# Optimization experiments

Measured on AMD Instinct MI355X. Metric: run time of the kernel, lower is better.

The kernel has to match this reference:

```python
import jax, jax.numpy as jnp
import numpy as np

N_STATE = 1024
N_HEAD = 16
HEAD_DIM = N_STATE // N_HEAD
SEQLENS = [1024, 896, 768, 640, 512, 384, 896, 1024]  # sum = 6144
TOTAL = sum(SEQLENS)


def setup_inputs() -> dict:
    key = jax.random.key(0)
    ks = jax.random.split(key, 8)
    s = 0.02
    cu = jnp.asarray(np.concatenate([[0], np.cumsum(SEQLENS)]), dtype=jnp.int32)
    return {
        "x": jax.random.normal(ks[0], (TOTAL, N_STATE), jnp.float32),
        "cu_seqlens": cu,
        "Wq": jax.random.normal(ks[1], (N_STATE, N_STATE), jnp.float32) * s,
        "bq": jax.random.normal(ks[2], (N_STATE,), jnp.float32) * s,
        "Wk": jax.random.normal(ks[3], (N_STATE, N_STATE), jnp.float32) * s,
        "Wv": jax.random.normal(ks[4], (N_STATE, N_STATE), jnp.float32) * s,
        "bv": jax.random.normal(ks[5], (N_STATE,), jnp.float32) * s,
        "Wo": jax.random.normal(ks[6], (N_STATE, N_STATE), jnp.float32) * s,
        "bo": jax.random.normal(ks[7], (N_STATE,), jnp.float32) * s,
    }


def reference(x, cu_seqlens, Wq, bq, Wk, Wv, bv, Wo, bo):
    # cu_seqlens is a static (host) quantity in the original (used via .tolist())
    cu = np.asarray(jax.device_get(cu_seqlens))
    seqlens = cu[1:] - cu[:-1]
    B = len(seqlens)
    Lmax = int(seqlens.max())

    q = x @ Wq.T + bq              # [T, n_state]
    k = x @ Wk.T                   # key has no bias
    v = x @ Wv.T + bv

    # static pad/unpad index maps (honoring the ragged structure)
    ar = np.arange(Lmax)
    valid = ar[None, :] < seqlens[:, None]             # [B, Lmax]
    idx = np.where(valid, cu[:-1, None] + ar[None, :], 0)
    unpad_idx = np.nonzero(valid.reshape(-1))[0]       # flat positions of real tokens
    valid_j = jnp.asarray(valid)

    def pad(t):  # [T, n_state] -> [B, Lmax, H, D], zeros in padding
        p = jnp.where(valid_j[:, :, None], t[idx], 0.0)
        return p.reshape(B, Lmax, N_HEAD, HEAD_DIM)

    qp, kp, vp = pad(q), pad(k), pad(v)
    scale = HEAD_DIM ** -0.5
    # torch adds the bool mask (True->1.0) after masked_fill(mask==0, -max):
    # valid keys get +1.0 (softmax-invariant shift), invalid keys get -finfo.max
    big_neg = jnp.finfo(x.dtype).max
    add_mask = jnp.where(valid_j, 1.0, -big_neg)[:, None, None, :]  # [B,1,1,Lmax]

    scores = jnp.einsum("bqhd,bkhd->bhqk", qp, kp) * scale + add_mask
    weights = jax.nn.softmax(scores, axis=-1)
    ctx = jnp.einsum("bhqk,bkhd->bqhd", weights, vp)   # [B, Lmax, H, D]
    ctx_flat = ctx.reshape(B * Lmax, N_STATE)[unpad_idx]  # [T, n_state]
    return ctx_flat @ Wo.T + bo
```

## Files before the change

kernel.cpp:

```cpp
#include <hip/hip_runtime.h>

typedef unsigned short u16;
typedef unsigned int u32;
typedef __attribute__((ext_vector_type(8))) short bf16x8;
typedef __attribute__((ext_vector_type(4))) float f32x4;

#define MFMA_BF16(a, b, c) __builtin_amdgcn_mfma_f32_16x16x32_bf16((a), (b), (c), 0, 0, 0)

#define QSCALE 0.18033688011112042f

__device__ __forceinline__ u16 f2bf(float f) {
    union { float f; unsigned u; } v; v.f = f;
    return (u16)((v.u + 0x7FFFu + ((v.u >> 16) & 1u)) >> 16);
}

__device__ __forceinline__ u32 pkbf(float a, float b) {
    union { float f; unsigned u; } x, y; x.f = a; y.f = b;
    return ((x.u + 0x8000u) >> 16) | ((y.u + 0x8000u) & 0xFFFF0000u);
}

__device__ __forceinline__ void async16(const void* g, void* l) {
    __builtin_amdgcn_global_load_lds(
        (const __attribute__((address_space(1))) void*)g,
        (__attribute__((address_space(3))) void*)l, 16, 0, 0);
}

__global__ __launch_bounds__(256) void cvt_kernel(const float* __restrict__ src,
                                                  u16* __restrict__ dst, int n4) {
    int i = blockIdx.x * 256 + threadIdx.x;
    if (i >= n4) return;
    float4 v = ((const float4*)src)[i];
    unsigned long long pk = (unsigned long long)f2bf(v.x)
                          | ((unsigned long long)f2bf(v.y) << 16)
                          | ((unsigned long long)f2bf(v.z) << 32)
                          | ((unsigned long long)f2bf(v.w) << 48);
    *(unsigned long long*)(dst + (size_t)i * 4) = pk;
}

__global__ __launch_bounds__(256) void cvt4_kernel(
    const float* __restrict__ a, const float* __restrict__ b,
    const float* __restrict__ c, const float* __restrict__ d,
    u16* __restrict__ oa, u16* __restrict__ ob, u16* __restrict__ oc, u16* __restrict__ od) {
    const float* src; u16* dst;
    switch (blockIdx.y) {
        case 0: src = a; dst = oa; break;
        case 1: src = b; dst = ob; break;
        case 2: src = c; dst = oc; break;
        default: src = d; dst = od; break;
    }
    int i = blockIdx.x * 256 + threadIdx.x;
    float4 v = ((const float4*)src)[i];
    unsigned long long pk = (unsigned long long)f2bf(v.x)
                          | ((unsigned long long)f2bf(v.y) << 16)
                          | ((unsigned long long)f2bf(v.z) << 32)
                          | ((unsigned long long)f2bf(v.w) << 48);
    *(unsigned long long*)(dst + (size_t)i * 4) = pk;
}

__global__ __launch_bounds__(256) void gemm_qkv(
    const u16* __restrict__ xb,
    const u16* __restrict__ Wqb, const u16* __restrict__ Wkb, const u16* __restrict__ Wvb,
    const float* __restrict__ bq, const float* __restrict__ bv,
    u16* __restrict__ qb, u16* __restrict__ kb, u16* __restrict__ vbT) {
    __shared__ __align__(16) u16 As[128 * 32];
    __shared__ __align__(16) u16 Bs[128 * 32];
    const int tid = threadIdx.x;
    const int m0 = blockIdx.x << 7;
    const int by = blockIdx.y;
    const int buf = by >> 3;
    const int n0 = (by & 7) << 7;
    const u16* __restrict__ W = (buf == 0) ? Wqb : (buf == 1) ? Wkb : Wvb;

    const int srow = tid >> 2;
    const int scg = tid & 3;
    const int wv = tid >> 6, lane = tid & 63, g = lane >> 4, c = lane & 15;
    const int wm = (wv & 1) << 6, wn = (wv >> 1) << 6;

    f32x4 zero = {0.f, 0.f, 0.f, 0.f};
    f32x4 acc[4][4];
#pragma unroll
    for (int i = 0; i < 4; ++i)
#pragma unroll
        for (int j = 0; j < 4; ++j) acc[i][j] = zero;

    for (int kt = 0; kt < 32; ++kt) {
        const int k0 = kt << 5;
        __syncthreads();
#pragma unroll
        for (int r = 0; r < 2; ++r) {
            int row = (r << 6) + srow;
            int gc = k0 + ((scg ^ ((row >> 2) & 3)) << 3);
            async16(xb + (size_t)(m0 + row) * 1024 + gc, As + (r << 11) + tid * 8);
            async16(W + (size_t)(n0 + row) * 1024 + gc, Bs + (r << 11) + tid * 8);
        }
        __syncthreads();
        bf16x8 af[4], bb[4];
#pragma unroll
        for (int i = 0; i < 4; ++i) {
            int ra = wm + (i << 4) + c;
            af[i] = *(const bf16x8*)(As + ra * 32 + ((g ^ ((ra >> 2) & 3)) << 3));
            int rb = wn + (i << 4) + c;
            bb[i] = *(const bf16x8*)(Bs + rb * 32 + ((g ^ ((rb >> 2) & 3)) << 3));
        }
#pragma unroll
        for (int i = 0; i < 4; ++i)
#pragma unroll
            for (int j = 0; j < 4; ++j) acc[i][j] = MFMA_BF16(af[i], bb[j], acc[i][j]);
    }

    if (buf == 0) {
#pragma unroll
        for (int j = 0; j < 4; ++j) {
            int col = n0 + wn + (j << 4) + c;
            float bias = bq[col];
#pragma unroll
            for (int i = 0; i < 4; ++i) {
                int rowb = m0 + wm + (i << 4) + (g << 2);
#pragma unroll
                for (int r = 0; r < 4; ++r)
                    qb[(size_t)(rowb + r) * 1024 + col] = f2bf((acc[i][j][r] + bias) * QSCALE);
            }
        }
    } else if (buf == 1) {
#pragma unroll
        for (int j = 0; j < 4; ++j) {
            int col = n0 + wn + (j << 4) + c;
#pragma unroll
            for (int i = 0; i < 4; ++i) {
                int rowb = m0 + wm + (i << 4) + (g << 2);
#pragma unroll
                for (int r = 0; r < 4; ++r)
                    kb[(size_t)(rowb + r) * 1024 + col] = f2bf(acc[i][j][r]);
            }
        }
    } else {
#pragma unroll
        for (int j = 0; j < 4; ++j) {
            int col = n0 + wn + (j << 4) + c;
            float bias = bv[col];
#pragma unroll
            for (int i = 0; i < 4; ++i) {
                int trow = m0 + wm + (i << 4) + (g << 2);
                unsigned long long pk =
                      (unsigned long long)f2bf(acc[i][j][0] + bias)
                    | ((unsigned long long)f2bf(acc[i][j][1] + bias) << 16)
                    | ((unsigned long long)f2bf(acc[i][j][2] + bias) << 32)
                    | ((unsigned long long)f2bf(acc[i][j][3] + bias) << 48);
                *(unsigned long long*)(vbT + (size_t)col * 6144 + trow) = pk;
            }
        }
    }
}

__global__ __launch_bounds__(256) void gemm_out(
    const u16* __restrict__ ctxb, const u16* __restrict__ Wob,
    const float* __restrict__ bo, float* __restrict__ out) {
    __shared__ __align__(16) u16 As[128 * 32];
    __shared__ __align__(16) u16 Bs[128 * 32];
    const int tid = threadIdx.x;
    const int m0 = blockIdx.x << 7;
    const int n0 = blockIdx.y << 7;
    const int srow = tid >> 2, scg = tid & 3;
    const int wv = tid >> 6, lane = tid & 63, g = lane >> 4, c = lane & 15;
    const int wm = (wv & 1) << 6, wn = (wv >> 1) << 6;

    f32x4 zero = {0.f, 0.f, 0.f, 0.f};
    f32x4 acc[4][4];
#pragma unroll
    for (int i = 0; i < 4; ++i)
#pragma unroll
        for (int j = 0; j < 4; ++j) acc[i][j] = zero;

    for (int kt = 0; kt < 32; ++kt) {
        const int k0 = kt << 5;
        __syncthreads();
#pragma unroll
        for (int r = 0; r < 2; ++r) {
            int row = (r << 6) + srow;
            int gc = k0 + ((scg ^ ((row >> 2) & 3)) << 3);
            async16(ctxb + (size_t)(m0 + row) * 1024 + gc, As + (r << 11) + tid * 8);
            async16(Wob + (size_t)(n0 + row) * 1024 + gc, Bs + (r << 11) + tid * 8);
        }
        __syncthreads();
        bf16x8 af[4], bb[4];
#pragma unroll
        for (int i = 0; i < 4; ++i) {
            int ra = wm + (i << 4) + c;
            af[i] = *(const bf16x8*)(As + ra * 32 + ((g ^ ((ra >> 2) & 3)) << 3));
            int rb = wn + (i << 4) + c;
            bb[i] = *(const bf16x8*)(Bs + rb * 32 + ((g ^ ((rb >> 2) & 3)) << 3));
        }
#pragma unroll
        for (int i = 0; i < 4; ++i)
#pragma unroll
            for (int j = 0; j < 4; ++j) acc[i][j] = MFMA_BF16(af[i], bb[j], acc[i][j]);
    }

#pragma unroll
    for (int j = 0; j < 4; ++j) {
        int col = n0 + wn + (j << 4) + c;
        float bias = bo[col];
#pragma unroll
        for (int i = 0; i < 4; ++i) {
            int rowb = m0 + wm + (i << 4) + (g << 2);
#pragma unroll
            for (int r = 0; r < 4; ++r)
                out[(size_t)(rowb + r) * 1024 + col] = acc[i][j][r] + bias;
        }
    }
}

__global__ __launch_bounds__(256) void attn_kernel(const u16* __restrict__ qb,
                                                   const u16* __restrict__ kb,
                                                   const u16* __restrict__ vbT,
                                                   u16* __restrict__ ctxb) {
    __shared__ __align__(16) u16 Ks[128 * 64];
    __shared__ __align__(16) u16 Vs[64 * 128];
    __shared__ __align__(16) u16 Ps[4 * 2048];

    const int tid = threadIdx.x;
    const int h = blockIdx.y;
    const int q0 = blockIdx.x << 6;

    const int cuv[9] = {0, 1024, 1920, 2688, 3328, 3840, 4224, 5120, 6144};
    int s0 = 0, e0 = 6144;
#pragma unroll
    for (int i = 1; i < 8; ++i) {
        if (q0 >= cuv[i]) s0 = cuv[i];
        if (q0 < cuv[i] && cuv[i] < e0) e0 = cuv[i];
    }
    const int ntiles = (e0 - s0) >> 7;

    const int wv = tid >> 6, lane = tid & 63, g = lane >> 4, c = lane & 15;
    const int wrow = wv << 4;

    {
        const int rr = tid >> 3, cg = tid & 7;
#pragma unroll
        for (int r = 0; r < 2; ++r) {
            int row = (r << 5) + rr;
            async16(qb + (size_t)(q0 + row) * 1024 + (h << 6) + ((cg ^ (row & 7)) << 3),
                    Ps + (r << 11) + tid * 8);
        }
    }
    __syncthreads();

    bf16x8 qf[2];
#pragma unroll
    for (int ks = 0; ks < 2; ++ks) {
        int row = wrow + c;
        qf[ks] = *(const bf16x8*)(Ps + row * 64 + ((((ks << 2) + g) ^ (row & 7)) << 3));
    }

    float m_run = -1e30f, l_run = 0.f;
    f32x4 zero = {0.f, 0.f, 0.f, 0.f};
    f32x4 oacc[4];
#pragma unroll
    for (int nt = 0; nt < 4; ++nt) oacc[nt] = zero;

    const int pbase = (wv << 11) + c * 128;
    const int c7 = c & 7;

    for (int kt = 0; kt < ntiles; ++kt) {
        const int kv0 = s0 + (kt << 7);
        __syncthreads();
        {
            const int rr = tid >> 3, cg = tid & 7;
#pragma unroll
            for (int r = 0; r < 4; ++r) {
                int row = (r << 5) + rr;
                async16(kb + (size_t)(kv0 + row) * 1024 + (h << 6) + ((cg ^ (row & 7)) << 3),
                        Ks + (r << 11) + tid * 8);
            }
            const int rr2 = tid >> 4, cg2 = tid & 15;
#pragma unroll
            for (int r = 0; r < 4; ++r) {
                int row = (r << 4) + rr2;
                async16(vbT + (size_t)((h << 6) + row) * 6144 + kv0 + ((cg2 ^ (row & 15)) << 3),
                        Vs + (r << 11) + tid * 8);
            }
        }
        __syncthreads();

        f32x4 st[8];
#pragma unroll
        for (int mt = 0; mt < 8; ++mt) st[mt] = zero;
#pragma unroll
        for (int mt = 0; mt < 8; ++mt) {
            int row = (mt << 4) + c;
            int sw = row & 7;
#pragma unroll
            for (int ks = 0; ks < 2; ++ks) {
                bf16x8 kf = *(const bf16x8*)(Ks + row * 64 + ((((ks << 2) + g) ^ sw) << 3));
                st[mt] = MFMA_BF16(kf, qf[ks], st[mt]);
            }
        }

        float mx = st[0][0];
#pragma unroll
        for (int mt = 0; mt < 8; ++mt)
#pragma unroll
            for (int r = 0; r < 4; ++r) mx = fmaxf(mx, st[mt][r]);
        mx = fmaxf(mx, __shfl_xor(mx, 16, 64));
        mx = fmaxf(mx, __shfl_xor(mx, 32, 64));
        float mnew = fmaxf(m_run, mx);
        float alpha = exp2f(m_run - mnew);
        m_run = mnew;

        float rsum = 0.f;
#pragma unroll
        for (int mt = 0; mt < 8; ++mt) {
            float p0 = exp2f(st[mt][0] - mnew);
            float p1 = exp2f(st[mt][1] - mnew);
            float p2 = exp2f(st[mt][2] - mnew);
            float p3 = exp2f(st[mt][3] - mnew);
            rsum += (p0 + p1) + (p2 + p3);
            int ph = ((mt << 2) + g) ^ (c7 << 1);
            *(uint2*)(Ps + pbase + (ph << 2)) = make_uint2(pkbf(p0, p1), pkbf(p2, p3));
        }
        rsum += __shfl_xor(rsum, 16, 64);
        rsum += __shfl_xor(rsum, 32, 64);
        l_run = l_run * alpha + rsum;

        float al[4];
#pragma unroll
        for (int r = 0; r < 4; ++r) al[r] = __shfl(alpha, (g << 2) + r, 16);
#pragma unroll
        for (int nt = 0; nt < 4; ++nt)
#pragma unroll
            for (int r = 0; r < 4; ++r) oacc[nt][r] *= al[r];

#pragma unroll
        for (int ks = 0; ks < 4; ++ks) {
            int pg = ((ks << 2) + g) ^ c7;
            bf16x8 pf = *(const bf16x8*)(Ps + pbase + (pg << 3));
#pragma unroll
            for (int nt = 0; nt < 4; ++nt) {
                int vrow = (nt << 4) + c;
                bf16x8 vf = *(const bf16x8*)(Vs + vrow * 128 + ((((ks << 2) + g) ^ (vrow & 15)) << 3));
                oacc[nt] = MFMA_BF16(pf, vf, oacc[nt]);
            }
        }
    }

    float inv = 1.0f / l_run;
    float invr[4];
#pragma unroll
    for (int r = 0; r < 4; ++r) invr[r] = __shfl(inv, (g << 2) + r, 16);
#pragma unroll
    for (int r = 0; r < 4; ++r) {
        size_t rowoff = (size_t)(q0 + wrow + (g << 2) + r) * 1024 + (h << 6);
#pragma unroll
        for (int nt = 0; nt < 4; ++nt)
            ctxb[rowoff + (nt << 4) + c] = f2bf(oacc[nt][r] * invr[r]);
    }
}

extern "C" void kernel_launch(void* const* d_in, const int* in_sizes, int n_in,
                              void* d_out, int out_size, void* d_ws, size_t ws_size,
                              hipStream_t stream) {
    const float* x  = (const float*)d_in[0];
    const float* Wq = (const float*)d_in[2];
    const float* bq = (const float*)d_in[3];
    const float* Wk = (const float*)d_in[4];
    const float* Wv = (const float*)d_in[5];
    const float* bv = (const float*)d_in[6];
    const float* Wo = (const float*)d_in[7];
    const float* bo = (const float*)d_in[8];
    float* out = (float*)d_out;

    u16* ws = (u16*)d_ws;
    u16* xb   = ws;
    u16* Wqb  = xb + 6291456;
    u16* Wkb  = Wqb + 1048576;
    u16* Wvb  = Wkb + 1048576;
    u16* Wob  = Wvb + 1048576;
    u16* qb   = Wob + 1048576;
    u16* kb   = qb + 6291456;
    u16* vbT  = kb + 6291456;
    u16* ctxb = xb;

    cvt_kernel<<<6144, 256, 0, stream>>>(x, xb, 1572864);
    cvt4_kernel<<<dim3(1024, 4), 256, 0, stream>>>(Wq, Wk, Wv, Wo, Wqb, Wkb, Wvb, Wob);

    gemm_qkv<<<dim3(48, 24), 256, 0, stream>>>(xb, Wqb, Wkb, Wvb, bq, bv, qb, kb, vbT);
    attn_kernel<<<dim3(96, 16), 256, 0, stream>>>(qb, kb, vbT, ctxb);
    gemm_out<<<dim3(48, 8), 256, 0, stream>>>(ctxb, Wob, bo, out);
}
```

Before: 249.8 us.

## Double-buffer LDS tiles in GEMMs and attention, merge conversion kernels

Adds ping-pong LDS buffers to both GEMM kernels and the attention kernel. The next K-tile (or K/V tile) is prefetched with async global-to-LDS loads while the current tile is consumed, which removes one barrier per iteration and hides load latency. The two fp32-to-bf16 conversion kernels become a single launch, and the GEMM LDS swizzle pattern is changed to use row>>1. The cost is doubled LDS use, notably about 80KB in attention, which may reduce occupancy.

```diff
diff --git a/kernel.cpp b/kernel.cpp
--- a/kernel.cpp
+++ b/kernel.cpp
@@ -25,10 +25,19 @@
         (__attribute__((address_space(3))) void*)l, 16, 0, 0);
 }
 
-__global__ __launch_bounds__(256) void cvt_kernel(const float* __restrict__ src,
-                                                  u16* __restrict__ dst, int n4) {
-    int i = blockIdx.x * 256 + threadIdx.x;
-    if (i >= n4) return;
+__global__ __launch_bounds__(256) void cvt_all(
+    const float* __restrict__ x, const float* __restrict__ Wq, const float* __restrict__ Wk,
+    const float* __restrict__ Wv, const float* __restrict__ Wo,
+    u16* __restrict__ xb, u16* __restrict__ Wqb, u16* __restrict__ Wkb,
+    u16* __restrict__ Wvb, u16* __restrict__ Wob) {
+    int b = blockIdx.x;
+    const float* src; u16* dst; int base;
+    if (b < 6144)      { src = x;  dst = xb;  base = b; }
+    else if (b < 7168) { src = Wq; dst = Wqb; base = b - 6144; }
+    else if (b < 8192) { src = Wk; dst = Wkb; base = b - 7168; }
+    else if (b < 9216) { src = Wv; dst = Wvb; base = b - 8192; }
+    else               { src = Wo; dst = Wob; base = b - 9216; }
+    int i = base * 256 + threadIdx.x;
     float4 v = ((const float4*)src)[i];
     unsigned long long pk = (unsigned long long)f2bf(v.x)
                           | ((unsigned long long)f2bf(v.y) << 16)
@@ -37,33 +46,13 @@
     *(unsigned long long*)(dst + (size_t)i * 4) = pk;
 }
 
-__global__ __launch_bounds__(256) void cvt4_kernel(
-    const float* __restrict__ a, const float* __restrict__ b,
-    const float* __restrict__ c, const float* __restrict__ d,
-    u16* __restrict__ oa, u16* __restrict__ ob, u16* __restrict__ oc, u16* __restrict__ od) {
-    const float* src; u16* dst;
-    switch (blockIdx.y) {
-        case 0: src = a; dst = oa; break;
-        case 1: src = b; dst = ob; break;
-        case 2: src = c; dst = oc; break;
-        default: src = d; dst = od; break;
-    }
-    int i = blockIdx.x * 256 + threadIdx.x;
-    float4 v = ((const float4*)src)[i];
-    unsigned long long pk = (unsigned long long)f2bf(v.x)
-                          | ((unsigned long long)f2bf(v.y) << 16)
-                          | ((unsigned long long)f2bf(v.z) << 32)
-                          | ((unsigned long long)f2bf(v.w) << 48);
-    *(unsigned long long*)(dst + (size_t)i * 4) = pk;
-}
-
 __global__ __launch_bounds__(256) void gemm_qkv(
     const u16* __restrict__ xb,
     const u16* __restrict__ Wqb, const u16* __restrict__ Wkb, const u16* __restrict__ Wvb,
     const float* __restrict__ bq, const float* __restrict__ bv,
     u16* __restrict__ qb, u16* __restrict__ kb, u16* __restrict__ vbT) {
-    __shared__ __align__(16) u16 As[128 * 32];
-    __shared__ __align__(16) u16 Bs[128 * 32];
+    __shared__ __align__(16) u16 As[2][128 * 32];
+    __shared__ __align__(16) u16 Bs[2][128 * 32];
     const int tid = threadIdx.x;
     const int m0 = blockIdx.x << 7;
     const int by = blockIdx.y;
@@ -76,6 +65,13 @@
     const int wv = tid >> 6, lane = tid & 63, g = lane >> 4, c = lane & 15;
     const int wm = (wv & 1) << 6, wn = (wv >> 1) << 6;
 
+    const u16* gA0 = xb + (size_t)(m0 + srow) * 1024;
+    const u16* gA1 = xb + (size_t)(m0 + 64 + srow) * 1024;
+    const u16* gB0 = W + (size_t)(n0 + srow) * 1024;
+    const u16* gB1 = W + (size_t)(n0 + 64 + srow) * 1024;
+    const int sw0 = (scg ^ ((srow >> 1) & 3)) << 3;
+    const int sw1 = (scg ^ (((srow + 64) >> 1) & 3)) << 3;
+
     f32x4 zero = {0.f, 0.f, 0.f, 0.f};
     f32x4 acc[4][4];
 #pragma unroll
@@ -83,24 +79,31 @@
 #pragma unroll
         for (int j = 0; j < 4; ++j) acc[i][j] = zero;
 
+    {
+        async16(gA0 + sw0, &As[0][tid * 8]);
+        async16(gB0 + sw0, &Bs[0][tid * 8]);
+        async16(gA1 + sw1, &As[0][2048 + tid * 8]);
+        async16(gB1 + sw1, &Bs[0][2048 + tid * 8]);
+    }
+
+#pragma unroll 2
     for (int kt = 0; kt < 32; ++kt) {
-        const int k0 = kt << 5;
+        const int cur = kt & 1;
         __syncthreads();
-#pragma unroll
-        for (int r = 0; r < 2; ++r) {
-            int row = (r << 6) + srow;
-            int gc = k0 + ((scg ^ ((row >> 2) & 3)) << 3);
-            async16(xb + (size_t)(m0 + row) * 1024 + gc, As + (r << 11) + tid * 8);
-            async16(W + (size_t)(n0 + row) * 1024 + gc, Bs + (r << 11) + tid * 8);
-        }
-        __syncthreads();
+        if (kt < 31) {
+            const int gc = ((kt + 1) << 5);
+            async16(gA0 + gc + sw0, &As[cur ^ 1][tid * 8]);
+            async16(gB0 + gc + sw0, &Bs[cur ^ 1][tid * 8]);
+            async16(gA1 + gc + sw1, &As[cur ^ 1][2048 + tid * 8]);
+            async16(gB1 + gc + sw1, &Bs[cur ^ 1][2048 + tid * 8]);
+        }
         bf16x8 af[4], bb[4];
 #pragma unroll
         for (int i = 0; i < 4; ++i) {
             int ra = wm + (i << 4) + c;
-            af[i] = *(const bf16x8*)(As + ra * 32 + ((g ^ ((ra >> 2) & 3)) << 3));
+            af[i] = *(const bf16x8*)(&As[cur][ra * 32 + ((g ^ ((ra >> 1) & 3)) << 3)]);
             int rb = wn + (i << 4) + c;
-            bb[i] = *(const bf16x8*)(Bs + rb * 32 + ((g ^ ((rb >> 2) & 3)) << 3));
+            bb[i] = *(const bf16x8*)(&Bs[cur][rb * 32 + ((g ^ ((rb >> 1) & 3)) << 3)]);
         }
 #pragma unroll
         for (int i = 0; i < 4; ++i)
@@ -155,8 +158,8 @@
 __global__ __launch_bounds__(256) void gemm_out(
     const u16* __restrict__ ctxb, const u16* __restrict__ Wob,
     const float* __restrict__ bo, float* __restrict__ out) {
-    __shared__ __align__(16) u16 As[128 * 32];
-    __shared__ __align__(16) u16 Bs[128 * 32];
+    __shared__ __align__(16) u16 As[2][128 * 32];
+    __shared__ __align__(16) u16 Bs[2][128 * 32];
     const int tid = threadIdx.x;
     const int m0 = blockIdx.x << 7;
     const int n0 = blockIdx.y << 7;
@@ -164,6 +167,13 @@
     const int wv = tid >> 6, lane = tid & 63, g = lane >> 4, c = lane & 15;
     const int wm = (wv & 1) << 6, wn = (wv >> 1) << 6;
 
+    const u16* gA0 = ctxb + (size_t)(m0 + srow) * 1024;
+    const u16* gA1 = ctxb + (size_t)(m0 + 64 + srow) * 1024;
+    const u16* gB0 = Wob + (size_t)(n0 + srow) * 1024;
+    const u16* gB1 = Wob + (size_t)(n0 + 64 + srow) * 1024;
+    const int sw0 = (scg ^ ((srow >> 1) & 3)) << 3;
+    const int sw1 = (scg ^ (((srow + 64) >> 1) & 3)) << 3;
+
     f32x4 zero = {0.f, 0.f, 0.f, 0.f};
     f32x4 acc[4][4];
 #pragma unroll
@@ -171,24 +181,31 @@
 #pragma unroll
         for (int j = 0; j < 4; ++j) acc[i][j] = zero;
 
+    {
+        async16(gA0 + sw0, &As[0][tid * 8]);
+        async16(gB0 + sw0, &Bs[0][tid * 8]);
+        async16(gA1 + sw1, &As[0][2048 + tid * 8]);
+        async16(gB1 + sw1, &Bs[0][2048 + tid * 8]);
+    }
+
+#pragma unroll 2
     for (int kt = 0; kt < 32; ++kt) {
-        const int k0 = kt << 5;
+        const int cur = kt & 1;
         __syncthreads();
-#pragma unroll
-        for (int r = 0; r < 2; ++r) {
-            int row = (r << 6) + srow;
-            int gc = k0 + ((scg ^ ((row >> 2) & 3)) << 3);
-            async16(ctxb + (size_t)(m0 + row) * 1024 + gc, As + (r << 11) + tid * 8);
-            async16(Wob + (size_t)(n0 + row) * 1024 + gc, Bs + (r << 11) + tid * 8);
-        }
-        __syncthreads();
+        if (kt < 31) {
+            const int gc = ((kt + 1) << 5);
+            async16(gA0 + gc + sw0, &As[cur ^ 1][tid * 8]);
+            async16(gB0 + gc + sw0, &Bs[cur ^ 1][tid * 8]);
+            async16(gA1 + gc + sw1, &As[cur ^ 1][2048 + tid * 8]);
+            async16(gB1 + gc + sw1, &Bs[cur ^ 1][2048 + tid * 8]);
+        }
         bf16x8 af[4], bb[4];
 #pragma unroll
         for (int i = 0; i < 4; ++i) {
             int ra = wm + (i << 4) + c;
-            af[i] = *(const bf16x8*)(As + ra * 32 + ((g ^ ((ra >> 2) & 3)) << 3));
+            af[i] = *(const bf16x8*)(&As[cur][ra * 32 + ((g ^ ((ra >> 1) & 3)) << 3)]);
             int rb = wn + (i << 4) + c;
-            bb[i] = *(const bf16x8*)(Bs + rb * 32 + ((g ^ ((rb >> 2) & 3)) << 3));
+            bb[i] = *(const bf16x8*)(&Bs[cur][rb * 32 + ((g ^ ((rb >> 1) & 3)) << 3)]);
         }
 #pragma unroll
         for (int i = 0; i < 4; ++i)
@@ -214,8 +231,8 @@
                                                    const u16* __restrict__ kb,
                                                    const u16* __restrict__ vbT,
                                                    u16* __restrict__ ctxb) {
-    __shared__ __align__(16) u16 Ks[128 * 64];
-    __shared__ __align__(16) u16 Vs[64 * 128];
+    __shared__ __align__(16) u16 Ks[2][128 * 64];
+    __shared__ __align__(16) u16 Vs[2][64 * 128];
     __shared__ __align__(16) u16 Ps[4 * 2048];
 
     const int tid = threadIdx.x;
@@ -234,14 +251,28 @@
     const int wv = tid >> 6, lane = tid & 63, g = lane >> 4, c = lane & 15;
     const int wrow = wv << 4;
 
+    const int rr = tid >> 3, cg = tid & 7;
+    const int rr2 = tid >> 4, cg2 = tid & 15;
+
     {
-        const int rr = tid >> 3, cg = tid & 7;
 #pragma unroll
         for (int r = 0; r < 2; ++r) {
             int row = (r << 5) + rr;
             async16(qb + (size_t)(q0 + row) * 1024 + (h << 6) + ((cg ^ (row & 7)) << 3),
                     Ps + (r << 11) + tid * 8);
         }
+#pragma unroll
+        for (int r = 0; r < 4; ++r) {
+            int row = (r << 5) + rr;
+            async16(kb + (size_t)(s0 + row) * 1024 + (h << 6) + ((cg ^ (row & 7)) << 3),
+                    &Ks[0][(r << 11) + tid * 8]);
+        }
+#pragma unroll
+        for (int r = 0; r < 4; ++r) {
+            int row = (r << 4) + rr2;
+            async16(vbT + (size_t)((h << 6) + row) * 6144 + s0 + ((cg2 ^ (row & 15)) << 3),
+                    &Vs[0][(r << 11) + tid * 8]);
+        }
     }
     __syncthreads();
 
@@ -262,25 +293,23 @@
     const int c7 = c & 7;
 
     for (int kt = 0; kt < ntiles; ++kt) {
-        const int kv0 = s0 + (kt << 7);
+        const int cur = kt & 1;
         __syncthreads();
-        {
-            const int rr = tid >> 3, cg = tid & 7;
+        if (kt + 1 < ntiles) {
+            const int kv1 = s0 + ((kt + 1) << 7);
 #pragma unroll
             for (int r = 0; r < 4; ++r) {
                 int row = (r << 5) + rr;
-                async16(kb + (size_t)(kv0 + row) * 1024 + (h << 6) + ((cg ^ (row & 7)) << 3),
-                        Ks + (r << 11) + tid * 8);
-            }
-            const int rr2 = tid >> 4, cg2 = tid & 15;
+                async16(kb + (size_t)(kv1 + row) * 1024 + (h << 6) + ((cg ^ (row & 7)) << 3),
+                        &Ks[cur ^ 1][(r << 11) + tid * 8]);
+            }
 #pragma unroll
             for (int r = 0; r < 4; ++r) {
                 int row = (r << 4) + rr2;
-                async16(vbT + (size_t)((h << 6) + row) * 6144 + kv0 + ((cg2 ^ (row & 15)) << 3),
-                        Vs + (r << 11) + tid * 8);
-            }
-        }
-        __syncthreads();
+                async16(vbT + (size_t)((h << 6) + row) * 6144 + kv1 + ((cg2 ^ (row & 15)) << 3),
+                        &Vs[cur ^ 1][(r << 11) + tid * 8]);
+            }
+        }
 
         f32x4 st[8];
 #pragma unroll
@@ -291,7 +320,7 @@
             int sw = row & 7;
 #pragma unroll
             for (int ks = 0; ks < 2; ++ks) {
-                bf16x8 kf = *(const bf16x8*)(Ks + row * 64 + ((((ks << 2) + g) ^ sw) << 3));
+                bf16x8 kf = *(const bf16x8*)(&Ks[cur][row * 64 + ((((ks << 2) + g) ^ sw) << 3)]);
                 st[mt] = MFMA_BF16(kf, qf[ks], st[mt]);
             }
         }
@@ -337,7 +366,7 @@
 #pragma unroll
             for (int nt = 0; nt < 4; ++nt) {
                 int vrow = (nt << 4) + c;
-                bf16x8 vf = *(const bf16x8*)(Vs + vrow * 128 + ((((ks << 2) + g) ^ (vrow & 15)) << 3));
+                bf16x8 vf = *(const bf16x8*)(&Vs[cur][vrow * 128 + ((((ks << 2) + g) ^ (vrow & 15)) << 3)]);
                 oacc[nt] = MFMA_BF16(pf, vf, oacc[nt]);
             }
         }
@@ -380,9 +409,7 @@
     u16* vbT  = kb + 6291456;
     u16* ctxb = xb;
 
-    cvt_kernel<<<6144, 256, 0, stream>>>(x, xb, 1572864);
-    cvt4_kernel<<<dim3(1024, 4), 256, 0, stream>>>(Wq, Wk, Wv, Wo, Wqb, Wkb, Wvb, Wob);
-
+    cvt_all<<<10240, 256, 0, stream>>>(x, Wq, Wk, Wv, Wo, xb, Wqb, Wkb, Wvb, Wob);
     gemm_qkv<<<dim3(48, 24), 256, 0, stream>>>(xb, Wqb, Wkb, Wvb, bq, bv, qb, kb, vbT);
     attn_kernel<<<dim3(96, 16), 256, 0, stream>>>(qb, kb, vbT, ctxb);
     gemm_out<<<dim3(48, 8), 256, 0, stream>>>(ctxb, Wob, bo, out);
```

Measured after the change: 260.2 us. 4.2% more time.

## Merge conversion kernels, deepen GEMM K-tile to 64, shrink output GEMM tiles

Applied to the files above, without the earlier changes.

Combines the x and weight fp32-to-bf16 conversions into one launch. Both GEMMs now stage a 64-wide K slice per iteration with an 8-way XOR swizzle and precomputed global pointers, which halves the barrier count per K loop. The output projection switches from 128x128 to 64x64 tiles, giving 1536 blocks instead of 384 so all CUs are busy, at the cost of less data reuse per block. The QKV GEMM doubles its LDS footprint, which may lower occupancy.

```diff
diff --git a/kernel.cpp b/kernel.cpp
--- a/kernel.cpp
+++ b/kernel.cpp
@@ -25,10 +25,19 @@
         (__attribute__((address_space(3))) void*)l, 16, 0, 0);
 }
 
-__global__ __launch_bounds__(256) void cvt_kernel(const float* __restrict__ src,
-                                                  u16* __restrict__ dst, int n4) {
-    int i = blockIdx.x * 256 + threadIdx.x;
-    if (i >= n4) return;
+__global__ __launch_bounds__(256) void cvt_all(
+    const float* __restrict__ x, const float* __restrict__ Wq, const float* __restrict__ Wk,
+    const float* __restrict__ Wv, const float* __restrict__ Wo,
+    u16* __restrict__ xb, u16* __restrict__ Wqb, u16* __restrict__ Wkb,
+    u16* __restrict__ Wvb, u16* __restrict__ Wob) {
+    int b = blockIdx.x;
+    const float* src; u16* dst; int base;
+    if (b < 6144)      { src = x;  dst = xb;  base = b; }
+    else if (b < 7168) { src = Wq; dst = Wqb; base = b - 6144; }
+    else if (b < 8192) { src = Wk; dst = Wkb; base = b - 7168; }
+    else if (b < 9216) { src = Wv; dst = Wvb; base = b - 8192; }
+    else               { src = Wo; dst = Wob; base = b - 9216; }
+    int i = base * 256 + threadIdx.x;
     float4 v = ((const float4*)src)[i];
     unsigned long long pk = (unsigned long long)f2bf(v.x)
                           | ((unsigned long long)f2bf(v.y) << 16)
@@ -37,33 +46,13 @@
     *(unsigned long long*)(dst + (size_t)i * 4) = pk;
 }
 
-__global__ __launch_bounds__(256) void cvt4_kernel(
-    const float* __restrict__ a, const float* __restrict__ b,
-    const float* __restrict__ c, const float* __restrict__ d,
-    u16* __restrict__ oa, u16* __restrict__ ob, u16* __restrict__ oc, u16* __restrict__ od) {
-    const float* src; u16* dst;
-    switch (blockIdx.y) {
-        case 0: src = a; dst = oa; break;
-        case 1: src = b; dst = ob; break;
-        case 2: src = c; dst = oc; break;
-        default: src = d; dst = od; break;
-    }
-    int i = blockIdx.x * 256 + threadIdx.x;
-    float4 v = ((const float4*)src)[i];
-    unsigned long long pk = (unsigned long long)f2bf(v.x)
-                          | ((unsigned long long)f2bf(v.y) << 16)
-                          | ((unsigned long long)f2bf(v.z) << 32)
-                          | ((unsigned long long)f2bf(v.w) << 48);
-    *(unsigned long long*)(dst + (size_t)i * 4) = pk;
-}
-
 __global__ __launch_bounds__(256) void gemm_qkv(
     const u16* __restrict__ xb,
     const u16* __restrict__ Wqb, const u16* __restrict__ Wkb, const u16* __restrict__ Wvb,
     const float* __restrict__ bq, const float* __restrict__ bv,
     u16* __restrict__ qb, u16* __restrict__ kb, u16* __restrict__ vbT) {
-    __shared__ __align__(16) u16 As[128 * 32];
-    __shared__ __align__(16) u16 Bs[128 * 32];
+    __shared__ __align__(16) u16 As[128 * 64];
+    __shared__ __align__(16) u16 Bs[128 * 64];
     const int tid = threadIdx.x;
     const int m0 = blockIdx.x << 7;
     const int by = blockIdx.y;
@@ -71,11 +60,19 @@
     const int n0 = (by & 7) << 7;
     const u16* __restrict__ W = (buf == 0) ? Wqb : (buf == 1) ? Wkb : Wvb;
 
-    const int srow = tid >> 2;
-    const int scg = tid & 3;
+    const int rr = tid >> 3;
+    const int cg = tid & 7;
     const int wv = tid >> 6, lane = tid & 63, g = lane >> 4, c = lane & 15;
     const int wm = (wv & 1) << 6, wn = (wv >> 1) << 6;
 
+    const int sw = (cg ^ (rr & 7)) << 3;
+    const u16* gA[4]; const u16* gB[4];
+#pragma unroll
+    for (int r = 0; r < 4; ++r) {
+        gA[r] = xb + (size_t)(m0 + (r << 5) + rr) * 1024 + sw;
+        gB[r] = W + (size_t)(n0 + (r << 5) + rr) * 1024 + sw;
+    }
+
     f32x4 zero = {0.f, 0.f, 0.f, 0.f};
     f32x4 acc[4][4];
 #pragma unroll
@@ -83,29 +80,30 @@
 #pragma unroll
         for (int j = 0; j < 4; ++j) acc[i][j] = zero;
 
-    for (int kt = 0; kt < 32; ++kt) {
-        const int k0 = kt << 5;
-        __syncthreads();
-#pragma unroll
-        for (int r = 0; r < 2; ++r) {
-            int row = (r << 6) + srow;
-            int gc = k0 + ((scg ^ ((row >> 2) & 3)) << 3);
-            async16(xb + (size_t)(m0 + row) * 1024 + gc, As + (r << 11) + tid * 8);
-            async16(W + (size_t)(n0 + row) * 1024 + gc, Bs + (r << 11) + tid * 8);
-        }
-        __syncthreads();
-        bf16x8 af[4], bb[4];
-#pragma unroll
-        for (int i = 0; i < 4; ++i) {
-            int ra = wm + (i << 4) + c;
-            af[i] = *(const bf16x8*)(As + ra * 32 + ((g ^ ((ra >> 2) & 3)) << 3));
-            int rb = wn + (i << 4) + c;
-            bb[i] = *(const bf16x8*)(Bs + rb * 32 + ((g ^ ((rb >> 2) & 3)) << 3));
-        }
-#pragma unroll
-        for (int i = 0; i < 4; ++i)
-#pragma unroll
-            for (int j = 0; j < 4; ++j) acc[i][j] = MFMA_BF16(af[i], bb[j], acc[i][j]);
+    for (int kt = 0; kt < 16; ++kt) {
+        const int k0 = kt << 6;
+        __syncthreads();
+#pragma unroll
+        for (int r = 0; r < 4; ++r) {
+            async16(gA[r] + k0, &As[(r << 11) + tid * 8]);
+            async16(gB[r] + k0, &Bs[(r << 11) + tid * 8]);
+        }
+        __syncthreads();
+#pragma unroll
+        for (int ks = 0; ks < 2; ++ks) {
+            bf16x8 af[4], bb[4];
+#pragma unroll
+            for (int i = 0; i < 4; ++i) {
+                int ra = wm + (i << 4) + c;
+                af[i] = *(const bf16x8*)(&As[ra * 64 + ((((ks << 2) + g) ^ (ra & 7)) << 3)]);
+                int rb = wn + (i << 4) + c;
+                bb[i] = *(const bf16x8*)(&Bs[rb * 64 + ((((ks << 2) + g) ^ (rb & 7)) << 3)]);
+            }
+#pragma unroll
+            for (int i = 0; i < 4; ++i)
+#pragma unroll
+                for (int j = 0; j < 4; ++j) acc[i][j] = MFMA_BF16(af[i], bb[j], acc[i][j]);
+        }
     }
 
     if (buf == 0) {
@@ -155,53 +153,62 @@
 __global__ __launch_bounds__(256) void gemm_out(
     const u16* __restrict__ ctxb, const u16* __restrict__ Wob,
     const float* __restrict__ bo, float* __restrict__ out) {
-    __shared__ __align__(16) u16 As[128 * 32];
-    __shared__ __align__(16) u16 Bs[128 * 32];
+    __shared__ __align__(16) u16 As[64 * 64];
+    __shared__ __align__(16) u16 Bs[64 * 64];
     const int tid = threadIdx.x;
-    const int m0 = blockIdx.x << 7;
-    const int n0 = blockIdx.y << 7;
-    const int srow = tid >> 2, scg = tid & 3;
+    const int m0 = blockIdx.x << 6;
+    const int n0 = blockIdx.y << 6;
+    const int rr = tid >> 3, cg = tid & 7;
     const int wv = tid >> 6, lane = tid & 63, g = lane >> 4, c = lane & 15;
-    const int wm = (wv & 1) << 6, wn = (wv >> 1) << 6;
+    const int wm = (wv & 1) << 5, wn = (wv >> 1) << 5;
+
+    const int sw = (cg ^ (rr & 7)) << 3;
+    const u16* gA[2]; const u16* gB[2];
+#pragma unroll
+    for (int r = 0; r < 2; ++r) {
+        gA[r] = ctxb + (size_t)(m0 + (r << 5) + rr) * 1024 + sw;
+        gB[r] = Wob + (size_t)(n0 + (r << 5) + rr) * 1024 + sw;
+    }
 
     f32x4 zero = {0.f, 0.f, 0.f, 0.f};
-    f32x4 acc[4][4];
-#pragma unroll
-    for (int i = 0; i < 4; ++i)
-#pragma unroll
-        for (int j = 0; j < 4; ++j) acc[i][j] = zero;
-
-    for (int kt = 0; kt < 32; ++kt) {
-        const int k0 = kt << 5;
+    f32x4 acc[2][2];
+#pragma unroll
+    for (int i = 0; i < 2; ++i)
+#pragma unroll
+        for (int j = 0; j < 2; ++j) acc[i][j] = zero;
+
+    for (int kt = 0; kt < 16; ++kt) {
+        const int k0 = kt << 6;
         __syncthreads();
 #pragma unroll
         for (int r = 0; r < 2; ++r) {
-            int row = (r << 6) + srow;
-            int gc = k0 + ((scg ^ ((row >> 2) & 3)) << 3);
-            async16(ctxb + (size_t)(m0 + row) * 1024 + gc, As + (r << 11) + tid * 8);
-            async16(Wob + (size_t)(n0 + row) * 1024 + gc, Bs + (r << 11) + tid * 8);
-        }
-        __syncthreads();
-        bf16x8 af[4], bb[4];
-#pragma unroll
-        for (int i = 0; i < 4; ++i) {
-            int ra = wm + (i << 4) + c;
-            af[i] = *(const bf16x8*)(As + ra * 32 + ((g ^ ((ra >> 2) & 3)) << 3));
-            int rb = wn + (i << 4) + c;
-            bb[i] = *(const bf16x8*)(Bs + rb * 32 + ((g ^ ((rb >> 2) & 3)) << 3));
-        }
-#pragma unroll
-        for (int i = 0; i < 4; ++i)
-#pragma unroll
-            for (int j = 0; j < 4; ++j) acc[i][j] = MFMA_BF16(af[i], bb[j], acc[i][j]);
-    }
-
-#pragma unroll
-    for (int j = 0; j < 4; ++j) {
+            async16(gA[r] + k0, &As[(r << 11) + tid * 8]);
+            async16(gB[r] + k0, &Bs[(r << 11) + tid * 8]);
+        }
+        __syncthreads();
+#pragma unroll
+        for (int ks = 0; ks < 2; ++ks) {
+            bf16x8 af[2], bb[2];
+#pragma unroll
+            for (int i = 0; i < 2; ++i) {
+                int ra = wm + (i << 4) + c;
+                af[i] = *(const bf16x8*)(&As[ra * 64 + ((((ks << 2) + g) ^ (ra & 7)) << 3)]);
+                int rb = wn + (i << 4) + c;
+                bb[i] = *(const bf16x8*)(&Bs[rb * 64 + ((((ks << 2) + g) ^ (rb & 7)) << 3)]);
+            }
+#pragma unroll
+            for (int i = 0; i < 2; ++i)
+#pragma unroll
+                for (int j = 0; j < 2; ++j) acc[i][j] = MFMA_BF16(af[i], bb[j], acc[i][j]);
+        }
+    }
+
+#pragma unroll
+    for (int j = 0; j < 2; ++j) {
         int col = n0 + wn + (j << 4) + c;
         float bias = bo[col];
 #pragma unroll
-        for (int i = 0; i < 4; ++i) {
+        for (int i = 0; i < 2; ++i) {
             int rowb = m0 + wm + (i << 4) + (g << 2);
 #pragma unroll
             for (int r = 0; r < 4; ++r)
@@ -291,7 +298,7 @@
             int sw = row & 7;
 #pragma unroll
             for (int ks = 0; ks < 2; ++ks) {
-                bf16x8 kf = *(const bf16x8*)(Ks + row * 64 + ((((ks << 2) + g) ^ sw) << 3));
+                bf16x8 kf = *(const bf16x8*)(&Ks[row * 64 + ((((ks << 2) + g) ^ sw) << 3)]);
                 st[mt] = MFMA_BF16(kf, qf[ks], st[mt]);
             }
         }
@@ -337,7 +344,7 @@
 #pragma unroll
             for (int nt = 0; nt < 4; ++nt) {
                 int vrow = (nt << 4) + c;
-                bf16x8 vf = *(const bf16x8*)(Vs + vrow * 128 + ((((ks << 2) + g) ^ (vrow & 15)) << 3));
+                bf16x8 vf = *(const bf16x8*)(&Vs[vrow * 128 + ((((ks << 2) + g) ^ (vrow & 15)) << 3)]);
                 oacc[nt] = MFMA_BF16(pf, vf, oacc[nt]);
             }
         }
@@ -380,10 +387,8 @@
     u16* vbT  = kb + 6291456;
     u16* ctxb = xb;
 
-    cvt_kernel<<<6144, 256, 0, stream>>>(x, xb, 1572864);
-    cvt4_kernel<<<dim3(1024, 4), 256, 0, stream>>>(Wq, Wk, Wv, Wo, Wqb, Wkb, Wvb, Wob);
-
+    cvt_all<<<10240, 256, 0, stream>>>(x, Wq, Wk, Wv, Wo, xb, Wqb, Wkb, Wvb, Wob);
     gemm_qkv<<<dim3(48, 24), 256, 0, stream>>>(xb, Wqb, Wkb, Wvb, bq, bv, qb, kb, vbT);
     attn_kernel<<<dim3(96, 16), 256, 0, stream>>>(qb, kb, vbT, ctxb);
-    gemm_out<<<dim3(48, 8), 256, 0, stream>>>(ctxb, Wob, bo, out);
-}
+    gemm_out<<<dim3(96, 16), 256, 0, stream>>>(ctxb, Wob, bo, out);
+}
```

Result: faster. 236.7 us (-5.2%).
